# Optimization experiments

Hardware: AMD Instinct MI355X
Metric: run time of the kernel (lower is better)

Reference implementation:

```python
import jax, jax.numpy as jnp
import numpy as np
import math

EMBED = 1024
HEADS = 16
HEAD_DIM = EMBED // HEADS


def setup_inputs() -> dict:
    key = jax.random.key(0)
    ks = jax.random.split(key, 6)
    scale = 1.0 / math.sqrt(EMBED)
    x = jax.random.normal(ks[0], (4, 2048, EMBED), dtype=jnp.float32)
    Wv = jax.random.normal(ks[1], (EMBED, EMBED), dtype=jnp.float32) * scale
    Wk = jax.random.normal(ks[2], (EMBED, EMBED), dtype=jnp.float32) * scale
    Wq = jax.random.normal(ks[3], (EMBED, EMBED), dtype=jnp.float32) * scale
    Wo = jax.random.normal(ks[4], (EMBED, EMBED), dtype=jnp.float32) * scale
    bo = jax.random.normal(ks[5], (EMBED,), dtype=jnp.float32) * 0.02
    return {"x": x, "Wq": Wq, "Wk": Wk, "Wv": Wv, "Wo": Wo, "bo": bo}


def reference(x, Wq, Wk, Wv, Wo, bo):
    N, S, E = x.shape
    H, D = HEADS, HEAD_DIM
    # Linear(E,E,bias=False): y = x @ W.T ; weights here stored as [out,in]
    q = (x @ Wq.T).reshape(N, S, H, D)
    k = (x @ Wk.T).reshape(N, S, H, D)
    v = (x @ Wv.T).reshape(N, S, H, D)
    energy = jnp.einsum('nqhd,nkhd->nhqk', q, k)  # [N,H,S,S]
    attn = jax.nn.softmax(energy / math.sqrt(D), axis=-1)
    out = jnp.einsum('nhql,nlhd->nqhd', attn, v).reshape(N, S, E)
    return out @ Wo.T + bo
```

## Files before the change

kernel.cpp:

```cpp
#include <hip/hip_runtime.h>
#include <stdint.h>

#define NB   4
#define SLEN 2048
#define EMB  1024
#define NH   16
#define HD   64
#define MTOT (NB * SLEN)

typedef __bf16 bf8_t  __attribute__((ext_vector_type(8)));
typedef __bf16 bf4_t  __attribute__((ext_vector_type(4)));
typedef float  f4_t   __attribute__((ext_vector_type(4)));

#if __has_builtin(__builtin_amdgcn_exp2f)
#define EXP2(x) __builtin_amdgcn_exp2f(x)
#else
#define EXP2(x) exp2f(x)
#endif

__device__ __forceinline__ void gld16(const void* g, void* l) {
    __builtin_amdgcn_global_load_lds(
        (__attribute__((address_space(1))) void*)(g),
        (__attribute__((address_space(3))) void*)(l),
        16, 0, 0);
}

__device__ __forceinline__ uint32_t pack_bf16_rtn(float a, float b) {
    uint32_t ua = __builtin_bit_cast(uint32_t, a) + 0x8000u;
    uint32_t ub = __builtin_bit_cast(uint32_t, b) + 0x8000u;
    return __builtin_amdgcn_perm(ub, ua, 0x07060302u);
}
__device__ __forceinline__ uint32_t pack_bf16_rtz(float a, float b) {
    return __builtin_amdgcn_perm(__builtin_bit_cast(uint32_t, b),
                                 __builtin_bit_cast(uint32_t, a), 0x07060302u);
}

__global__ __launch_bounds__(256) void cast_f2b(const float* __restrict__ s,
                                                __bf16* __restrict__ d, int n) {
    int i = (blockIdx.x * 256 + threadIdx.x) * 4;
    if (i >= n) return;
    float4 f = *(const float4*)(s + i);
    bf4_t o = { (__bf16)f.x, (__bf16)f.y, (__bf16)f.z, (__bf16)f.w };
    *(bf4_t*)(d + i) = o;
}

__global__ __launch_bounds__(256) void cast_w4(const float* __restrict__ Wq,
                                               const float* __restrict__ Wk,
                                               const float* __restrict__ Wv,
                                               const float* __restrict__ Wo,
                                               __bf16* __restrict__ d) {
    int y = blockIdx.y;
    const float* s = (y == 0) ? Wq : (y == 1) ? Wk : (y == 2) ? Wv : Wo;
    int i = (blockIdx.x * 256 + threadIdx.x) * 4;
    float4 f = *(const float4*)(s + i);
    bf4_t o = { (__bf16)f.x, (__bf16)f.y, (__bf16)f.z, (__bf16)f.w };
    *(bf4_t*)(d + (size_t)y * (EMB * EMB) + i) = o;
}

template <int MODE>
__global__ __launch_bounds__(256) void gemm_bt(const __bf16* __restrict__ A,
                                               const __bf16* __restrict__ B,
                                               void* __restrict__ Cv,
                                               const float* __restrict__ bias,
                                               int M, int N, int K) {
    __shared__ __bf16 As[128 * 64];
    __shared__ __bf16 Bs[128 * 64];

    const int tid  = threadIdx.x;
    const int lane = tid & 63;
    const int w    = tid >> 6;
    const int quad = lane >> 4;
    const int l16  = lane & 15;
    const int m0   = blockIdx.x * 128;
    const int n0   = blockIdx.y * 128;
    const int wm   = (w >> 1) * 64;
    const int wn   = (w & 1) * 64;

    f4_t acc[4][4];
#pragma unroll
    for (int i = 0; i < 4; ++i)
#pragma unroll
        for (int j = 0; j < 4; ++j) acc[i][j] = (f4_t){0.f, 0.f, 0.f, 0.f};

    for (int k0 = 0; k0 < K; k0 += 64) {
        __syncthreads();
#pragma unroll
        for (int t = 0; t < 4; ++t) {
            int c   = t * 256 + tid;
            int row = c >> 3;
            int kc  = (c & 7) ^ (row & 7);
            int cb  = c & ~63;
            gld16(A + (size_t)(m0 + row) * K + k0 + kc * 8, &As[cb * 8]);
            gld16(B + (size_t)(n0 + row) * K + k0 + kc * 8, &Bs[cb * 8]);
        }
        __syncthreads();
#pragma unroll
        for (int ks = 0; ks < 2; ++ks) {
            bf8_t af[4], bfr[4];
#pragma unroll
            for (int i = 0; i < 4; ++i) {
                int r = wm + i * 16 + l16;
                af[i] = *(const bf8_t*)&As[r * 64 + (((ks * 4 + quad) ^ (r & 7)) * 8)];
            }
#pragma unroll
            for (int j = 0; j < 4; ++j) {
                int r = wn + j * 16 + l16;
                bfr[j] = *(const bf8_t*)&Bs[r * 64 + (((ks * 4 + quad) ^ (r & 7)) * 8)];
            }
#pragma unroll
            for (int i = 0; i < 4; ++i)
#pragma unroll
                for (int j = 0; j < 4; ++j)
                    acc[i][j] = __builtin_amdgcn_mfma_f32_16x16x32_bf16(af[i], bfr[j],
                                                                        acc[i][j], 0, 0, 0);
        }
    }

#pragma unroll
    for (int i = 0; i < 4; ++i) {
#pragma unroll
        for (int j = 0; j < 4; ++j) {
            int m   = m0 + wm + i * 16 + quad * 4;
            int col = n0 + wn + j * 16 + l16;
            if (MODE == 2) {
                float* Cf = (float*)Cv;
#pragma unroll
                for (int r = 0; r < 4; ++r)
                    Cf[(size_t)(m + r) * N + col] = acc[i][j][r] + bias[col];
            } else {
                __bf16* qb = (__bf16*)Cv;
                if (n0 < 1024) {
#pragma unroll
                    for (int r = 0; r < 4; ++r)
                        qb[(size_t)(m + r) * 1024 + col] = (__bf16)acc[i][j][r];
                } else if (n0 < 2048) {
                    __bf16* kb = qb + (size_t)8 * 1024 * 1024;
#pragma unroll
                    for (int r = 0; r < 4; ++r)
                        kb[(size_t)(m + r) * 1024 + (col - 1024)] = (__bf16)acc[i][j][r];
                } else {
                    __bf16* vtb = qb + (size_t)16 * 1024 * 1024;
                    size_t idx = ((size_t)(m >> 11) * 1024 + (col - 2048)) * 2048 + (m & 2047);
                    bf4_t pk = { (__bf16)acc[i][j][0], (__bf16)acc[i][j][1],
                                 (__bf16)acc[i][j][2], (__bf16)acc[i][j][3] };
                    *(bf4_t*)&vtb[idx] = pk;
                }
            }
        }
    }
}

__global__ __launch_bounds__(256, 2) void attn_fwd(const __bf16* __restrict__ Q,
                                                   const __bf16* __restrict__ K,
                                                   const __bf16* __restrict__ Vt,
                                                   __bf16* __restrict__ O) {
    __shared__ __bf16 Ks[64 * 64];
    __shared__ __bf16 Vs[64 * 64];
    __shared__ __bf16 Ps[4 * 64 * 72];

    const int tid  = threadIdx.x;
    const int lane = tid & 63;
    const int w    = tid >> 6;
    const int quad = lane >> 4;
    const int l16  = lane & 15;
    const int nh   = blockIdx.y;
    const int n    = nh >> 4;
    const int h    = nh & 15;
    const int q0   = blockIdx.x * 256 + w * 64;

    const float QSCALE = 0.125f * 1.44269504f;

    bf8_t bq[4][2];
#pragma unroll
    for (int jq = 0; jq < 4; ++jq)
#pragma unroll
        for (int ks = 0; ks < 2; ++ks) {
            bf8_t v = *(const bf8_t*)(Q + (size_t)(n * SLEN + q0 + jq * 16 + l16) * EMB +
                                      h * HD + ks * 32 + quad * 8);
#pragma unroll
            for (int t = 0; t < 8; ++t) v[t] = (__bf16)((float)v[t] * QSCALE);
            bq[jq][ks] = v;
        }

    bf8_t aones;
#pragma unroll
    for (int t = 0; t < 8; ++t) aones[t] = (__bf16)1.0f;

    f4_t ls[4];
    f4_t o[4][4];
#pragma unroll
    for (int jq = 0; jq < 4; ++jq) {
        ls[jq] = (f4_t){0.f, 0.f, 0.f, 0.f};
#pragma unroll
        for (int jd = 0; jd < 4; ++jd) o[jq][jd] = (f4_t){0.f, 0.f, 0.f, 0.f};
    }

    const __bf16* kbase = K + (size_t)n * SLEN * EMB + h * HD;
    const __bf16* vbase = Vt + (size_t)nh * HD * SLEN;
    __bf16* pw = Ps + w * 64 * 72;
    const int sw = l16 & 7;

    for (int l0 = 0; l0 < SLEN; l0 += 64) {
        __syncthreads();
#pragma unroll
        for (int t = 0; t < 2; ++t) {
            int c   = t * 256 + tid;
            int row = c >> 3;
            int kc  = (c & 7) ^ (row & 7);
            int cb  = c & ~63;
            gld16(kbase + (size_t)(l0 + row) * EMB + kc * 8, &Ks[cb * 8]);
            gld16(vbase + (size_t)row * SLEN + l0 + kc * 8, &Vs[cb * 8]);
        }
        __syncthreads();

#pragma unroll
        for (int jk = 0; jk < 4; ++jk) {
            bf8_t ak[2];
#pragma unroll
            for (int ks = 0; ks < 2; ++ks)
                ak[ks] = *(const bf8_t*)&Ks[(jk * 16 + l16) * 64 +
                                            (((ks * 4 + quad) ^ sw) * 8)];
#pragma unroll
            for (int jq = 0; jq < 4; ++jq) {
                f4_t e = (f4_t){0.f, 0.f, 0.f, 0.f};
                e = __builtin_amdgcn_mfma_f32_16x16x32_bf16(ak[0], bq[jq][0], e, 0, 0, 0);
                e = __builtin_amdgcn_mfma_f32_16x16x32_bf16(ak[1], bq[jq][1], e, 0, 0, 0);
                uint32_t d0 = pack_bf16_rtz(EXP2(e[0]), EXP2(e[1]));
                uint32_t d1 = pack_bf16_rtz(EXP2(e[2]), EXP2(e[3]));
                *(uint2*)&pw[(jq * 16 + l16) * 72 + jk * 16 + quad * 4] =
                    (uint2){d0, d1};
            }
        }

#pragma unroll
        for (int ks = 0; ks < 2; ++ks) {
            bf8_t bp[4];
#pragma unroll
            for (int jq = 0; jq < 4; ++jq)
                bp[jq] = *(const bf8_t*)&pw[(jq * 16 + l16) * 72 + ks * 32 + quad * 8];
#pragma unroll
            for (int jq = 0; jq < 4; ++jq)
                ls[jq] = __builtin_amdgcn_mfma_f32_16x16x32_bf16(aones, bp[jq],
                                                                 ls[jq], 0, 0, 0);
#pragma unroll
            for (int jd = 0; jd < 4; ++jd) {
                bf8_t av = *(const bf8_t*)&Vs[(jd * 16 + l16) * 64 +
                                              (((ks * 4 + quad) ^ sw) * 8)];
#pragma unroll
                for (int jq = 0; jq < 4; ++jq)
                    o[jq][jd] = __builtin_amdgcn_mfma_f32_16x16x32_bf16(av, bp[jq],
                                                                        o[jq][jd], 0, 0, 0);
            }
        }
    }

#pragma unroll
    for (int jq = 0; jq < 4; ++jq) {
        float inv = 1.0f / ls[jq][0];
#pragma unroll
        for (int jd = 0; jd < 4; ++jd) {
            uint32_t d0 = pack_bf16_rtn(o[jq][jd][0] * inv, o[jq][jd][1] * inv);
            uint32_t d1 = pack_bf16_rtn(o[jq][jd][2] * inv, o[jq][jd][3] * inv);
            *(uint2*)&O[(size_t)(n * SLEN + q0 + jq * 16 + l16) * EMB + h * HD +
                        jd * 16 + quad * 4] = (uint2){d0, d1};
        }
    }
}

extern "C" void kernel_launch(void* const* d_in, const int* in_sizes, int n_in,
                              void* d_out, int out_size, void* d_ws, size_t ws_size,
                              hipStream_t stream) {
    const float* x  = (const float*)d_in[0];
    const float* Wq = (const float*)d_in[1];
    const float* Wk = (const float*)d_in[2];
    const float* Wv = (const float*)d_in[3];
    const float* Wo = (const float*)d_in[4];
    const float* bo = (const float*)d_in[5];

    char* wsb = (char*)d_ws;
    const size_t MB = (size_t)1 << 20;
    __bf16* xb  = (__bf16*)(wsb + 0 * MB);
    __bf16* ab  = xb;
    __bf16* wqb = (__bf16*)(wsb + 16 * MB);
    __bf16* wob = (__bf16*)(wsb + 22 * MB);
    __bf16* qb  = (__bf16*)(wsb + 24 * MB);
    __bf16* vtb = (__bf16*)(wsb + 56 * MB);

    const int NX = MTOT * EMB;
    const int NW = EMB * EMB;

    cast_f2b<<<dim3(NX / 1024), dim3(256), 0, stream>>>(x, xb, NX);
    cast_w4<<<dim3(NW / 1024, 4), dim3(256), 0, stream>>>(Wq, Wk, Wv, Wo, wqb);

    gemm_bt<3><<<dim3(MTOT / 128, 3072 / 128), 256, 0, stream>>>(
        xb, wqb, qb, nullptr, MTOT, 3072, EMB);

    attn_fwd<<<dim3(SLEN / 256, NB * NH), 256, 0, stream>>>(qb, qb + (size_t)8 * MB,
                                                            vtb, ab);

    gemm_bt<2><<<dim3(MTOT / 128, EMB / 128), 256, 0, stream>>>(
        ab, wob, d_out, bo, MTOT, EMB, EMB);
}
```

Before: 264.9 us.

## Double-buffer K/V tiles in attention and merge cast kernels into one launch

The attention kernel now keeps two LDS buffers for its K and V tiles. The async global-to-LDS load of the next tile is issued before computing on the current one, so memory latency can overlap the MFMA and exp work. The two fp32-to-bf16 cast kernels are merged into a single launch that picks its source by block index, saving one launch. In exchange, LDS use per block rises by 16 KB, and the compiler's waitcnt placement for the async LDS loads may still serialize the overlap.

```diff
diff --git a/kernel.cpp b/kernel.cpp
--- a/kernel.cpp
+++ b/kernel.cpp
@@ -35,26 +35,28 @@
                                  __builtin_bit_cast(uint32_t, a), 0x07060302u);
 }
 
-__global__ __launch_bounds__(256) void cast_f2b(const float* __restrict__ s,
-                                                __bf16* __restrict__ d, int n) {
-    int i = (blockIdx.x * 256 + threadIdx.x) * 4;
-    if (i >= n) return;
+__global__ __launch_bounds__(256) void cast_all(const float* __restrict__ x,
+                                                const float* __restrict__ Wq,
+                                                const float* __restrict__ Wk,
+                                                const float* __restrict__ Wv,
+                                                const float* __restrict__ Wo,
+                                                __bf16* __restrict__ xb,
+                                                __bf16* __restrict__ wb) {
+    int b = blockIdx.x;
+    const float* s;
+    __bf16* d;
+    if (b < 8192) {
+        s = x; d = xb;
+    } else {
+        int y = (b - 8192) >> 10;
+        s = (y == 0) ? Wq : (y == 1) ? Wk : (y == 2) ? Wv : Wo;
+        d = wb + (size_t)y * (EMB * EMB);
+        b = (b - 8192) & 1023;
+    }
+    int i = (b * 256 + (int)threadIdx.x) * 4;
     float4 f = *(const float4*)(s + i);
     bf4_t o = { (__bf16)f.x, (__bf16)f.y, (__bf16)f.z, (__bf16)f.w };
     *(bf4_t*)(d + i) = o;
-}
-
-__global__ __launch_bounds__(256) void cast_w4(const float* __restrict__ Wq,
-                                               const float* __restrict__ Wk,
-                                               const float* __restrict__ Wv,
-                                               const float* __restrict__ Wo,
-                                               __bf16* __restrict__ d) {
-    int y = blockIdx.y;
-    const float* s = (y == 0) ? Wq : (y == 1) ? Wk : (y == 2) ? Wv : Wo;
-    int i = (blockIdx.x * 256 + threadIdx.x) * 4;
-    float4 f = *(const float4*)(s + i);
-    bf4_t o = { (__bf16)f.x, (__bf16)f.y, (__bf16)f.z, (__bf16)f.w };
-    *(bf4_t*)(d + (size_t)y * (EMB * EMB) + i) = o;
 }
 
 template <int MODE>
@@ -150,12 +152,74 @@
     }
 }
 
+__device__ __forceinline__ void attn_stage(const __bf16* __restrict__ kbase,
+                                           const __bf16* __restrict__ vbase,
+                                           int l0, int tid,
+                                           __bf16* __restrict__ Ksb,
+                                           __bf16* __restrict__ Vsb) {
+#pragma unroll
+    for (int t = 0; t < 2; ++t) {
+        int c   = t * 256 + tid;
+        int row = c >> 3;
+        int kc  = (c & 7) ^ (row & 7);
+        int cb  = c & ~63;
+        gld16(kbase + (size_t)(l0 + row) * EMB + kc * 8, Ksb + cb * 8);
+        gld16(vbase + (size_t)row * SLEN + l0 + kc * 8, Vsb + cb * 8);
+    }
+}
+
+__device__ __forceinline__ void attn_tile(const __bf16* __restrict__ Ksb,
+                                          const __bf16* __restrict__ Vsb,
+                                          __bf16* __restrict__ pw,
+                                          const bf8_t (*bq)[2], bf8_t aones,
+                                          f4_t* ls, f4_t (*o)[4],
+                                          int quad, int l16, int sw) {
+#pragma unroll
+    for (int jk = 0; jk < 4; ++jk) {
+        bf8_t ak[2];
+#pragma unroll
+        for (int ks = 0; ks < 2; ++ks)
+            ak[ks] = *(const bf8_t*)&Ksb[(jk * 16 + l16) * 64 +
+                                         (((ks * 4 + quad) ^ sw) * 8)];
+#pragma unroll
+        for (int jq = 0; jq < 4; ++jq) {
+            f4_t e = (f4_t){0.f, 0.f, 0.f, 0.f};
+            e = __builtin_amdgcn_mfma_f32_16x16x32_bf16(ak[0], bq[jq][0], e, 0, 0, 0);
+            e = __builtin_amdgcn_mfma_f32_16x16x32_bf16(ak[1], bq[jq][1], e, 0, 0, 0);
+            uint32_t d0 = pack_bf16_rtz(EXP2(e[0]), EXP2(e[1]));
+            uint32_t d1 = pack_bf16_rtz(EXP2(e[2]), EXP2(e[3]));
+            *(uint2*)&pw[(jq * 16 + l16) * 72 + jk * 16 + quad * 4] = (uint2){d0, d1};
+        }
+    }
+#pragma unroll
+    for (int ks = 0; ks < 2; ++ks) {
+        bf8_t bp[4];
+#pragma unroll
+        for (int jq = 0; jq < 4; ++jq)
+            bp[jq] = *(const bf8_t*)&pw[(jq * 16 + l16) * 72 + ks * 32 + quad * 8];
+#pragma unroll
+        for (int jq = 0; jq < 4; ++jq)
+            ls[jq] = __builtin_amdgcn_mfma_f32_16x16x32_bf16(aones, bp[jq], ls[jq], 0, 0, 0);
+#pragma unroll
+        for (int jd = 0; jd < 4; ++jd) {
+            bf8_t av = *(const bf8_t*)&Vsb[(jd * 16 + l16) * 64 +
+                                           (((ks * 4 + quad) ^ sw) * 8)];
+#pragma unroll
+            for (int jq = 0; jq < 4; ++jq)
+                o[jq][jd] = __builtin_amdgcn_mfma_f32_16x16x32_bf16(av, bp[jq],
+                                                                    o[jq][jd], 0, 0, 0);
+        }
+    }
+}
+
 __global__ __launch_bounds__(256, 2) void attn_fwd(const __bf16* __restrict__ Q,
                                                    const __bf16* __restrict__ K,
                                                    const __bf16* __restrict__ Vt,
                                                    __bf16* __restrict__ O) {
-    __shared__ __bf16 Ks[64 * 64];
-    __shared__ __bf16 Vs[64 * 64];
+    __shared__ __bf16 Ks0[64 * 64];
+    __shared__ __bf16 Ks1[64 * 64];
+    __shared__ __bf16 Vs0[64 * 64];
+    __shared__ __bf16 Vs1[64 * 64];
     __shared__ __bf16 Ps[4 * 64 * 72];
 
     const int tid  = threadIdx.x;
@@ -200,58 +264,17 @@
     __bf16* pw = Ps + w * 64 * 72;
     const int sw = l16 & 7;
 
-    for (int l0 = 0; l0 < SLEN; l0 += 64) {
+    attn_stage(kbase, vbase, 0, tid, Ks0, Vs0);
+
+    for (int it = 0; it < 32; it += 2) {
+        int l0 = it * 64;
         __syncthreads();
-#pragma unroll
-        for (int t = 0; t < 2; ++t) {
-            int c   = t * 256 + tid;
-            int row = c >> 3;
-            int kc  = (c & 7) ^ (row & 7);
-            int cb  = c & ~63;
-            gld16(kbase + (size_t)(l0 + row) * EMB + kc * 8, &Ks[cb * 8]);
-            gld16(vbase + (size_t)row * SLEN + l0 + kc * 8, &Vs[cb * 8]);
-        }
+        attn_stage(kbase, vbase, l0 + 64, tid, Ks1, Vs1);
+        attn_tile(Ks0, Vs0, pw, bq, aones, ls, o, quad, l16, sw);
         __syncthreads();
-
-#pragma unroll
-        for (int jk = 0; jk < 4; ++jk) {
-            bf8_t ak[2];
-#pragma unroll
-            for (int ks = 0; ks < 2; ++ks)
-                ak[ks] = *(const bf8_t*)&Ks[(jk * 16 + l16) * 64 +
-                                            (((ks * 4 + quad) ^ sw) * 8)];
-#pragma unroll
-            for (int jq = 0; jq < 4; ++jq) {
-                f4_t e = (f4_t){0.f, 0.f, 0.f, 0.f};
-                e = __builtin_amdgcn_mfma_f32_16x16x32_bf16(ak[0], bq[jq][0], e, 0, 0, 0);
-                e = __builtin_amdgcn_mfma_f32_16x16x32_bf16(ak[1], bq[jq][1], e, 0, 0, 0);
-                uint32_t d0 = pack_bf16_rtz(EXP2(e[0]), EXP2(e[1]));
-                uint32_t d1 = pack_bf16_rtz(EXP2(e[2]), EXP2(e[3]));
-                *(uint2*)&pw[(jq * 16 + l16) * 72 + jk * 16 + quad * 4] =
-                    (uint2){d0, d1};
-            }
-        }
-
-#pragma unroll
-        for (int ks = 0; ks < 2; ++ks) {
-            bf8_t bp[4];
-#pragma unroll
-            for (int jq = 0; jq < 4; ++jq)
-                bp[jq] = *(const bf8_t*)&pw[(jq * 16 + l16) * 72 + ks * 32 + quad * 8];
-#pragma unroll
-            for (int jq = 0; jq < 4; ++jq)
-                ls[jq] = __builtin_amdgcn_mfma_f32_16x16x32_bf16(aones, bp[jq],
-                                                                 ls[jq], 0, 0, 0);
-#pragma unroll
-            for (int jd = 0; jd < 4; ++jd) {
-                bf8_t av = *(const bf8_t*)&Vs[(jd * 16 + l16) * 64 +
-                                              (((ks * 4 + quad) ^ sw) * 8)];
-#pragma unroll
-                for (int jq = 0; jq < 4; ++jq)
-                    o[jq][jd] = __builtin_amdgcn_mfma_f32_16x16x32_bf16(av, bp[jq],
-                                                                        o[jq][jd], 0, 0, 0);
-            }
-        }
+        int lnn = (l0 + 128 < SLEN) ? l0 + 128 : l0 + 64;
+        attn_stage(kbase, vbase, lnn, tid, Ks0, Vs0);
+        attn_tile(Ks1, Vs1, pw, bq, aones, ls, o, quad, l16, sw);
     }
 
 #pragma unroll
@@ -286,11 +309,7 @@
     __bf16* qb  = (__bf16*)(wsb + 24 * MB);
     __bf16* vtb = (__bf16*)(wsb + 56 * MB);
 
-    const int NX = MTOT * EMB;
-    const int NW = EMB * EMB;
-
-    cast_f2b<<<dim3(NX / 1024), dim3(256), 0, stream>>>(x, xb, NX);
-    cast_w4<<<dim3(NW / 1024, 4), dim3(256), 0, stream>>>(Wq, Wk, Wv, Wo, wqb);
+    cast_all<<<dim3(12288), dim3(256), 0, stream>>>(x, Wq, Wk, Wv, Wo, xb, wqb);
 
     gemm_bt<3><<<dim3(MTOT / 128, 3072 / 128), 256, 0, stream>>>(
         xb, wqb, qb, nullptr, MTOT, 3072, EMB);
```

New measurement: 262.9 us. Within noise of the previous version (-0.7%).
